# Kernel optimization log

Measured on AMD Instinct MI355X. Metric: run time of the kernel, lower is better.

The kernel has to match this reference:

```python
import jax, jax.numpy as jnp
import numpy as np

N_NODES = 100000
N_EDGES = 1600000
IN_CH = 128
DIM = 128
OUT_CH = 10
NUM_GRAPHS = 128
BN_EPS = 1e-5


def _bn_train(h, gamma, beta):
    # BatchNorm1d in training mode: batch statistics over the node axis
    mean = jnp.mean(h, axis=0)
    var = jnp.var(h, axis=0)
    return (h - mean) * jax.lax.rsqrt(var + BN_EPS) * gamma + beta


def _gin_conv(x, src, dst, W1, b1, gamma, beta, W2, b2):
    # GINConv with eps=0: nn(x + sum_{j in N(i)} x_j)
    agg = jax.ops.segment_sum(x[src], dst, num_segments=x.shape[0])  # [N, d]
    h = (x + agg) @ W1 + b1
    h = jax.nn.relu(_bn_train(h, gamma, beta))
    h = jax.nn.relu(h @ W2 + b2)
    return h


def setup_inputs() -> dict:
    key = jax.random.key(0)
    ks = jax.random.split(key, 16)
    s = 0.02
    inp = {
        "x": jax.random.normal(ks[0], (N_NODES, IN_CH), dtype=jnp.float32),
        "edge_index": jax.random.randint(ks[1], (2, N_EDGES), 0, N_NODES, dtype=jnp.int64),
        "batch": jnp.sort(jax.random.randint(ks[2], (N_NODES,), 0, NUM_GRAPHS, dtype=jnp.int64)),
        # conv1 MLP
        "W1a": jax.random.normal(ks[3], (IN_CH, DIM), dtype=jnp.float32) * s,
        "b1a": jnp.zeros((DIM,), jnp.float32),
        "ga": jnp.ones((DIM,), jnp.float32),
        "ba": jnp.zeros((DIM,), jnp.float32),
        "W2a": jax.random.normal(ks[4], (DIM, DIM), dtype=jnp.float32) * s,
        "b2a": jnp.zeros((DIM,), jnp.float32),
        # conv2 MLP
        "W1b": jax.random.normal(ks[5], (DIM, DIM), dtype=jnp.float32) * s,
        "b1b": jnp.zeros((DIM,), jnp.float32),
        "gb": jnp.ones((DIM,), jnp.float32),
        "bb": jnp.zeros((DIM,), jnp.float32),
        "W2b": jax.random.normal(ks[6], (DIM, DIM), dtype=jnp.float32) * s,
        "b2b": jnp.zeros((DIM,), jnp.float32),
        # readout linears
        "Wl1": jax.random.normal(ks[7], (DIM, DIM), dtype=jnp.float32) * s,
        "bl1": jnp.zeros((DIM,), jnp.float32),
        "Wl2": jax.random.normal(ks[8], (DIM, OUT_CH), dtype=jnp.float32) * s,
        "bl2": jnp.zeros((OUT_CH,), jnp.float32),
    }
    return inp


def reference(x, edge_index, batch, W1a, b1a, ga, ba, W2a, b2a,
              W1b, b1b, gb, bb, W2b, b2b, Wl1, bl1, Wl2, bl2):
    src, dst = edge_index[0], edge_index[1]
    h = _gin_conv(x, src, dst, W1a, b1a, ga, ba, W2a, b2a)
    h = _gin_conv(h, src, dst, W1b, b1b, gb, bb, W2b, b2b)
    pooled = jax.ops.segment_sum(h, batch, num_segments=NUM_GRAPHS)  # [G, d]
    out = jax.nn.relu(pooled @ Wl1 + bl1)
    # dropout p=0.5 is identity in deterministic/eval evaluation
    out = out @ Wl2 + bl2
    return out
```

## Files before the change

### kernel.cpp

```cpp
#include <hip/hip_runtime.h>

#define N_NODES    100000
#define N_EDGES    1600000
#define DIM        128
#define OUT_CH     10
#define NUM_GRAPHS 128
#define BN_EPS     1e-5f

#define BSHIFT   8
#define NB2      391
#define CAP2     5120
#define NTILES   782

typedef __attribute__((ext_vector_type(8))) short short8;
typedef __attribute__((ext_vector_type(4))) float floatx4;

__device__ inline float bf2f(unsigned short u) {
    union { unsigned i; float f; } v; v.i = (unsigned)u << 16; return v.f;
}
__device__ inline unsigned short f2bf(float f) {
    union { float f; unsigned i; } v; v.f = f;
    unsigned r = (v.i + 0x7fffu + ((v.i >> 16) & 1u)) >> 16;
    return (unsigned short)r;
}

__device__ inline void async_cp16(const unsigned short* g, unsigned short* l) {
    __builtin_amdgcn_global_load_lds(
        (const __attribute__((address_space(1))) void*)g,
        (__attribute__((address_space(3))) void*)l, 16, 0, 0);
}

__global__ void k_cvt_x(const float* __restrict__ x, unsigned short* __restrict__ xb,
                        int* __restrict__ gcur, float* __restrict__ stats4,
                        float* __restrict__ pooled) {
    int t = threadIdx.x;
    if (blockIdx.x == 0) {
        for (int i = t; i < NB2 + 1; i += 256) gcur[i] = 0;
        for (int i = t; i < 4 * DIM; i += 256) stats4[i] = 0.f;
        for (int i = t; i < NUM_GRAPHS * DIM; i += 256) pooled[i] = 0.f;
    }
    int idx = blockIdx.x * 256 + t;
    float4 v = ((const float4*)x)[idx];
    ushort4 o;
    o.x = f2bf(v.x); o.y = f2bf(v.y); o.z = f2bf(v.z); o.w = f2bf(v.w);
    ((ushort4*)xb)[idx] = o;
}

__global__ void k_prep_w(const float* __restrict__ W0, const float* __restrict__ W1,
                         const float* __restrict__ W2, const float* __restrict__ W3,
                         unsigned short* __restrict__ Wt) {
    const float* Ws[4] = {W0, W1, W2, W3};
    const float* W = Ws[blockIdx.y];
    unsigned short* o = Wt + blockIdx.y * (DIM * DIM);
    int idx = blockIdx.x * 256 + threadIdx.x;
    int n = idx >> 7, k = idx & 127;
    o[idx] = f2bf(W[k * DIM + n]);
}

__global__ __launch_bounds__(256)
void k_bucket(const int* __restrict__ src, const int* __restrict__ dst,
              int* __restrict__ gcur, unsigned* __restrict__ pairs) {
    __shared__ int cnt[NB2 + 1];
    __shared__ int lofs[NB2 + 1];
    __shared__ int gbase[NB2 + 1];
    __shared__ int scanA[256], scanB[256];
    __shared__ int stage[8192];

    int t = threadIdx.x;
    for (int i = t; i < NB2 + 1; i += 256) cnt[i] = 0;
    __syncthreads();
    int base = blockIdx.x * 8192;
    int n_e = min(8192, N_EDGES - base);
    for (int i = t; i < n_e; i += 256)
        atomicAdd(&cnt[dst[base + i] >> BSHIFT], 1);
    __syncthreads();
    int vA = cnt[t];
    int vB = (t < NB2 - 256) ? cnt[256 + t] : 0;
    scanA[t] = vA; scanB[t] = vB;
    __syncthreads();
    for (int off = 1; off < 256; off <<= 1) {
        int tA = (t >= off) ? scanA[t - off] : 0;
        int tB = (t >= off) ? scanB[t - off] : 0;
        __syncthreads();
        scanA[t] += tA; scanB[t] += tB;
        __syncthreads();
    }
    lofs[t] = scanA[t] - vA;
    if (t < NB2 - 256) lofs[256 + t] = scanA[255] + scanB[t] - vB;
    __syncthreads();
    for (int i = t; i < NB2; i += 256) {
        gbase[i] = (cnt[i] > 0) ? atomicAdd(&gcur[i], cnt[i]) : 0;
        cnt[i] = lofs[i];
    }
    __syncthreads();
    for (int i = t; i < n_e; i += 256) {
        int d = dst[base + i];
        int b = d >> BSHIFT;
        int pos = atomicAdd(&cnt[b], 1);
        stage[pos] = (int)(((unsigned)src[base + i] << 8) | (unsigned)(d & 255));
    }
    __syncthreads();
    int w = t >> 6, lane = t & 63;
    for (int b = w; b < NB2; b += 4) {
        int len = cnt[b] - lofs[b];
        int g0  = gbase[b];
        int maxlen = CAP2 - g0; if (maxlen < 0) maxlen = 0;
        if (len > maxlen) len = maxlen;
        unsigned* dp = pairs + (size_t)b * CAP2 + g0;
        const int* sp = stage + lofs[b];
        for (int i = lane; i < len; i += 64) dp[i] = (unsigned)sp[i];
    }
}

__global__ void k_bscan(const int* __restrict__ gcur, int* __restrict__ bbase,
                        int* __restrict__ row_ptr) {
    __shared__ int sh[512];
    int t = threadIdx.x;
    int v = (t < NB2) ? min(gcur[t], CAP2) : 0;
    sh[t] = v; __syncthreads();
    for (int off = 1; off < 512; off <<= 1) {
        int tmp = (t >= off) ? sh[t - off] : 0;
        __syncthreads();
        sh[t] += tmp;
        __syncthreads();
    }
    if (t < NB2) bbase[t] = sh[t] - v;
    if (t == NB2 - 1) { bbase[NB2] = sh[t]; row_ptr[N_NODES] = sh[t]; }
}

__global__ __launch_bounds__(256)
void k_csr(const unsigned* __restrict__ pairs, const int* __restrict__ gcur,
           const int* __restrict__ bbase, int* __restrict__ row_ptr,
           int* __restrict__ col) {
    __shared__ int hist[256];
    __shared__ int cur[256];
    __shared__ int stage[CAP2];
    int bi = blockIdx.x, t = threadIdx.x;
    hist[t] = 0; __syncthreads();
    int n = min(gcur[bi], CAP2);
    const unsigned* P = pairs + (size_t)bi * CAP2;
    for (int i = t; i < n; i += 256)
        atomicAdd(&hist[P[i] & 255u], 1);
    __syncthreads();
    int self = hist[t];
    cur[t] = self; __syncthreads();
    for (int off = 1; off < 256; off <<= 1) {
        int tmp = (t >= off) ? cur[t - off] : 0;
        __syncthreads();
        cur[t] += tmp;
        __syncthreads();
    }
    int excl = cur[t] - self;
    int base = bbase[bi];
    int node = (bi << 8) + t;
    if (node < N_NODES) row_ptr[node] = base + excl;
    cur[t] = excl;
    __syncthreads();
    for (int i = t; i < n; i += 256) {
        unsigned e = P[i];
        int pos = atomicAdd(&cur[e & 255u], 1);
        stage[pos] = (int)(e >> 8);
    }
    __syncthreads();
    for (int i = t; i < n; i += 256) col[base + i] = stage[i];
}

__global__ void k_agg(const unsigned short* __restrict__ X,
                      unsigned short* __restrict__ Out,
                      const int* __restrict__ row_ptr, const int* __restrict__ col) {
    int wid = (blockIdx.x * 256 + threadIdx.x) >> 6;
    if (wid >= N_NODES) return;
    int lane = threadIdx.x & 63;
    int half = lane >> 5, m = lane & 31;
    const ushort4* X4 = (const ushort4*)X;

    float a0=0.f,a1=0.f,a2=0.f,a3=0.f;
    float c0=0.f,c1=0.f,c2=0.f,c3=0.f;
    if (half == 0) {
        ushort4 sv = X4[(size_t)wid * 32 + m];
        a0 = bf2f(sv.x); a1 = bf2f(sv.y); a2 = bf2f(sv.z); a3 = bf2f(sv.w);
    }
    int s = row_ptr[wid], e = row_ptr[wid + 1];
    int p = s + half;
    for (; p + 6 < e; p += 8) {
        int n0 = col[p], n1 = col[p + 2], n2 = col[p + 4], n3 = col[p + 6];
        ushort4 v0 = X4[(size_t)n0 * 32 + m];
        ushort4 v1 = X4[(size_t)n1 * 32 + m];
        ushort4 v2 = X4[(size_t)n2 * 32 + m];
        ushort4 v3 = X4[(size_t)n3 * 32 + m];
        a0 += bf2f(v0.x); a1 += bf2f(v0.y); a2 += bf2f(v0.z); a3 += bf2f(v0.w);
        c0 += bf2f(v1.x); c1 += bf2f(v1.y); c2 += bf2f(v1.z); c3 += bf2f(v1.w);
        a0 += bf2f(v2.x); a1 += bf2f(v2.y); a2 += bf2f(v2.z); a3 += bf2f(v2.w);
        c0 += bf2f(v3.x); c1 += bf2f(v3.y); c2 += bf2f(v3.z); c3 += bf2f(v3.w);
    }
    for (; p < e; p += 2) {
        ushort4 v = X4[(size_t)col[p] * 32 + m];
        a0 += bf2f(v.x); a1 += bf2f(v.y); a2 += bf2f(v.z); a3 += bf2f(v.w);
    }
    a0 += c0; a1 += c1; a2 += c2; a3 += c3;
    a0 += __shfl_xor(a0, 32);
    a1 += __shfl_xor(a1, 32);
    a2 += __shfl_xor(a2, 32);
    a3 += __shfl_xor(a3, 32);
    if (half == 0) {
        ushort4 o;
        o.x = f2bf(a0); o.y = f2bf(a1); o.z = f2bf(a2); o.w = f2bf(a3);
        ((ushort4*)Out)[(size_t)wid * 32 + m] = o;
    }
}

template<bool BN_LOAD, bool STATS, bool RELU_ST>
__global__ __launch_bounds__(512)
void k_gemm(const unsigned short* __restrict__ In, unsigned short* __restrict__ Out,
            const unsigned short* __restrict__ Wt, const float* __restrict__ bias,
            const float* __restrict__ ssum_in, const float* __restrict__ ssq_in,
            const float* __restrict__ gamma, const float* __restrict__ beta,
            float* __restrict__ ssum_out, float* __restrict__ ssq_out) {
    __shared__ __align__(16) unsigned short sB[128 * 128];
    __shared__ float ssc[128], ssh[128];
    __shared__ float s_sum[128], s_sq[128];

    int t = threadIdx.x;
    int w = t >> 6, lane = t & 63;
    int tm = w >> 2, wv = w & 3;
    int m = lane & 15;
    int q = lane >> 4;
    int tile = blockIdx.x * 2 + tm;
    int r0 = tile * 128;

    int rowA0 = min(r0 + wv * 32 + m,      N_NODES - 1);
    int rowA1 = min(r0 + wv * 32 + 16 + m, N_NODES - 1);
    short8 a0[4], a1[4];
    #pragma unroll
    for (int kk = 0; kk < 4; ++kk) {
        a0[kk] = *(const short8*)(In + (size_t)rowA0 * 128 + kk * 32 + q * 8);
        a1[kk] = *(const short8*)(In + (size_t)rowA1 * 128 + kk * 32 + q * 8);
    }

    #pragma unroll
    for (int u = 0; u < 4; ++u) {
        int i = (w * 4 + u) * 64 + lane;
        int n = i >> 4, p = i & 15;
        async_cp16(Wt + n * 128 + ((p ^ (n & 7)) << 3), sB + (size_t)(w * 4 + u) * 512);
    }
    if (BN_LOAD && t < 128) {
        float mn  = ssum_in[t] * (1.0f / N_NODES);
        float var = ssq_in[t] * (1.0f / N_NODES) - mn * mn;
        float inv = rsqrtf(var + BN_EPS);
        float sc  = gamma[t] * inv;
        ssc[t] = sc; ssh[t] = beta[t] - mn * sc;
    }
    if (STATS && t < 128) { s_sum[t] = 0.f; s_sq[t] = 0.f; }
    __syncthreads();

    if (BN_LOAD) {
        #pragma unroll
        for (int kk = 0; kk < 4; ++kk) {
            int base = kk * 32 + q * 8;
            #pragma unroll
            for (int j = 0; j < 8; ++j) {
                float scj = ssc[base + j], shj = ssh[base + j];
                float f0 = fmaxf(bf2f((unsigned short)a0[kk][j]) * scj + shj, 0.f);
                float f1 = fmaxf(bf2f((unsigned short)a1[kk][j]) * scj + shj, 0.f);
                a0[kk][j] = (short)f2bf(f0);
                a1[kk][j] = (short)f2bf(f1);
            }
        }
    }

    int sw = m & 7;
    floatx4 acc[2][8] = {};
    #pragma unroll
    for (int kk = 0; kk < 4; ++kk) {
        int cp = (kk * 4 + q) ^ sw;
        #pragma unroll
        for (int c = 0; c < 8; ++c) {
            int nr = c * 16 + m;
            short8 b = *(const short8*)&sB[nr * 128 + (cp << 3)];
            acc[0][c] = __builtin_amdgcn_mfma_f32_16x16x32_bf16(b, a0[kk], acc[0][c], 0, 0, 0);
            acc[1][c] = __builtin_amdgcn_mfma_f32_16x16x32_bf16(b, a1[kk], acc[1][c], 0, 0, 0);
        }
    }

    #pragma unroll
    for (int c = 0; c < 8; ++c) {
        int ch0 = c * 16 + q * 4;
        float4 bv = *(const float4*)(bias + ch0);
        float sr[4] = {0,0,0,0}, qr[4] = {0,0,0,0};
        #pragma unroll
        for (int h = 0; h < 2; ++h) {
            int node = r0 + wv * 32 + h * 16 + m;
            float v0 = acc[h][c][0] + bv.x;
            float v1 = acc[h][c][1] + bv.y;
            float v2 = acc[h][c][2] + bv.z;
            float v3 = acc[h][c][3] + bv.w;
            if (RELU_ST) {
                v0 = fmaxf(v0, 0.f); v1 = fmaxf(v1, 0.f);
                v2 = fmaxf(v2, 0.f); v3 = fmaxf(v3, 0.f);
            }
            if (node < N_NODES) {
                ushort4 o;
                o.x = f2bf(v0); o.y = f2bf(v1); o.z = f2bf(v2); o.w = f2bf(v3);
                *(ushort4*)(Out + (size_t)node * 128 + ch0) = o;
                if (STATS) {
                    sr[0] += v0; sr[1] += v1; sr[2] += v2; sr[3] += v3;
                    qr[0] += v0*v0; qr[1] += v1*v1; qr[2] += v2*v2; qr[3] += v3*v3;
                }
            }
        }
        if (STATS) {
            #pragma unroll
            for (int msk = 1; msk <= 8; msk <<= 1) {
                #pragma unroll
                for (int r = 0; r < 4; ++r) {
                    sr[r] += __shfl_xor(sr[r], msk);
                    qr[r] += __shfl_xor(qr[r], msk);
                }
            }
            if (m == 0) {
                #pragma unroll
                for (int r = 0; r < 4; ++r) {
                    atomicAdd(&s_sum[ch0 + r], sr[r]);
                    atomicAdd(&s_sq [ch0 + r], qr[r]);
                }
            }
        }
    }
    if (STATS) {
        __syncthreads();
        if (t < 128) {
            atomicAdd(&ssum_out[t], s_sum[t]);
            atomicAdd(&ssq_out [t], s_sq[t]);
        }
    }
}

#define POOL_BLOCKS 512
#define POOL_CHUNK  196
__global__ void k_pool(const unsigned short* __restrict__ h, const int* __restrict__ batch,
                       float* __restrict__ pooled) {
    int c  = threadIdx.x;
    int n0 = blockIdx.x * POOL_CHUNK;
    if (n0 >= N_NODES) return;
    int n1 = min(n0 + POOL_CHUNK, N_NODES);
    int g = batch[n0];
    float acc = 0.f;
    for (int i = n0; i < n1; ++i) {
        int gi = batch[i];
        if (gi != g) { atomicAdd(&pooled[g * DIM + c], acc); acc = 0.f; g = gi; }
        acc += bf2f(h[(size_t)i * DIM + c]);
    }
    atomicAdd(&pooled[g * DIM + c], acc);
}

__global__ void k_readout(const float* __restrict__ pooled,
                          const float* __restrict__ Wl1, const float* __restrict__ bl1,
                          const float* __restrict__ Wl2, const float* __restrict__ bl2,
                          float* __restrict__ out) {
    __shared__ float p[128], r[128];
    int g = blockIdx.x, c = threadIdx.x;
    p[c] = pooled[g * DIM + c];
    __syncthreads();
    float s = bl1[c];
    #pragma unroll 8
    for (int k = 0; k < DIM; ++k) s += p[k] * Wl1[k * DIM + c];
    r[c] = fmaxf(s, 0.f);
    __syncthreads();
    if (c < OUT_CH) {
        float s2 = bl2[c];
        #pragma unroll 8
        for (int k = 0; k < DIM; ++k) s2 += r[k] * Wl2[k * OUT_CH + c];
        out[g * OUT_CH + c] = s2;
    }
}

extern "C" void kernel_launch(void* const* d_in, const int* in_sizes, int n_in,
                              void* d_out, int out_size, void* d_ws, size_t ws_size,
                              hipStream_t stream) {
    const float* x   = (const float*)d_in[0];
    const int*   ei  = (const int*)d_in[1];
    const int*   bat = (const int*)d_in[2];
    const float* W1a = (const float*)d_in[3];
    const float* b1a = (const float*)d_in[4];
    const float* ga  = (const float*)d_in[5];
    const float* ba  = (const float*)d_in[6];
    const float* W2a = (const float*)d_in[7];
    const float* b2a = (const float*)d_in[8];
    const float* W1b = (const float*)d_in[9];
    const float* b1b = (const float*)d_in[10];
    const float* gb  = (const float*)d_in[11];
    const float* bbt = (const float*)d_in[12];
    const float* W2b = (const float*)d_in[13];
    const float* b2b = (const float*)d_in[14];
    const float* Wl1 = (const float*)d_in[15];
    const float* bl1 = (const float*)d_in[16];
    const float* Wl2 = (const float*)d_in[17];
    const float* bl2 = (const float*)d_in[18];
    float* out = (float*)d_out;

    const int* src = ei;
    const int* dst = ei + N_EDGES;

    char* w = (char*)d_ws;
    size_t off = 0;
    auto alloc = [&](size_t bytes) -> char* {
        char* p = w + off; off += (bytes + 255) & ~(size_t)255; return p;
    };
    unsigned short* xb   = (unsigned short*)alloc((size_t)N_NODES * DIM * 2);
    unsigned short* nb0  = (unsigned short*)alloc((size_t)N_NODES * DIM * 2);
    unsigned short* nb1  = (unsigned short*)alloc((size_t)N_NODES * DIM * 2);
    unsigned short* Wtb  = (unsigned short*)alloc((size_t)4 * DIM * DIM * 2);
    unsigned* pairs = (unsigned*)alloc((size_t)NB2 * CAP2 * 4);
    int*   row_ptr = (int*)  alloc((size_t)(N_NODES + 1) * 4);
    int*   col     = (int*)  alloc((size_t)N_EDGES * 4);
    int*   gcur    = (int*)  alloc((NB2 + 1) * 4);
    int*   bbase   = (int*)  alloc((NB2 + 1) * 4);
    float* stats4  = (float*)alloc((size_t)4 * DIM * 4);
    float* pooled  = (float*)alloc((size_t)NUM_GRAPHS * DIM * 4);
    float* ssumA = stats4, *ssqA = stats4 + DIM, *ssumB = stats4 + 2*DIM, *ssqB = stats4 + 3*DIM;

    k_cvt_x<<<(N_NODES * DIM / 4) / 256, 256, 0, stream>>>(x, xb, gcur, stats4, pooled);
    k_prep_w<<<dim3(64, 4), 256, 0, stream>>>(W1a, W2a, W1b, W2b, Wtb);
    const unsigned short* Wt1a = Wtb;
    const unsigned short* Wt2a = Wtb + DIM * DIM;
    const unsigned short* Wt1b = Wtb + 2 * DIM * DIM;
    const unsigned short* Wt2b = Wtb + 3 * DIM * DIM;

    k_bucket<<<(N_EDGES + 8191) / 8192, 256, 0, stream>>>(src, dst, gcur, pairs);
    k_bscan<<<1, 512, 0, stream>>>(gcur, bbase, row_ptr);
    k_csr<<<NB2, 256, 0, stream>>>(pairs, gcur, bbase, row_ptr, col);

    int agg_blocks  = (N_NODES * 64) / 256;
    int gemm_blocks = NTILES / 2;

    k_agg<<<agg_blocks, 256, 0, stream>>>(xb, nb0, row_ptr, col);
    k_gemm<false, true, false><<<gemm_blocks, 512, 0, stream>>>(
        nb0, nb1, Wt1a, b1a, nullptr, nullptr, nullptr, nullptr, ssumA, ssqA);
    k_gemm<true, false, true><<<gemm_blocks, 512, 0, stream>>>(
        nb1, nb0, Wt2a, b2a, ssumA, ssqA, ga, ba, nullptr, nullptr);
    k_agg<<<agg_blocks, 256, 0, stream>>>(nb0, nb1, row_ptr, col);
    k_gemm<false, true, false><<<gemm_blocks, 512, 0, stream>>>(
        nb1, nb0, Wt1b, b1b, nullptr, nullptr, nullptr, nullptr, ssumB, ssqB);
    k_gemm<true, false, true><<<gemm_blocks, 512, 0, stream>>>(
        nb0, nb1, Wt2b, b2b, ssumB, ssqB, gb, bbt, nullptr, nullptr);
    k_pool<<<POOL_BLOCKS, 128, 0, stream>>>(nb1, bat, pooled);
    k_readout<<<NUM_GRAPHS, 128, 0, stream>>>(pooled, Wl1, bl1, Wl2, bl2, out);
}
```

Baseline: 495.9 us.

## Make GEMM kernel persistent with register prefetch of next tile

The row-tile GEMM becomes a persistent kernel: a fixed grid of 256 blocks of 256 threads loops over the 782 tiles. It loads the weight matrix into LDS once per block rather than once per two tiles, and prefetches the next tile's A rows into registers while computing the current one. This amortises the weight staging and overlaps global loads with MFMA work, at the cost of higher register pressure and fewer waves per block. The second half of the tail tiles may leave some CUs idle.

```diff
diff --git a/kernel.cpp b/kernel.cpp
--- a/kernel.cpp
+++ b/kernel.cpp
@@ -11,6 +11,7 @@
 #define NB2      391
 #define CAP2     5120
 #define NTILES   782
+#define GEMM_GRID 256
 
 typedef __attribute__((ext_vector_type(8))) short short8;
 typedef __attribute__((ext_vector_type(4))) float floatx4;
@@ -210,7 +211,7 @@
 }
 
 template<bool BN_LOAD, bool STATS, bool RELU_ST>
-__global__ __launch_bounds__(512)
+__global__ __launch_bounds__(256)
 void k_gemm(const unsigned short* __restrict__ In, unsigned short* __restrict__ Out,
             const unsigned short* __restrict__ Wt, const float* __restrict__ bias,
             const float* __restrict__ ssum_in, const float* __restrict__ ssq_in,
@@ -222,26 +223,15 @@
 
     int t = threadIdx.x;
     int w = t >> 6, lane = t & 63;
-    int tm = w >> 2, wv = w & 3;
     int m = lane & 15;
     int q = lane >> 4;
-    int tile = blockIdx.x * 2 + tm;
-    int r0 = tile * 128;
-
-    int rowA0 = min(r0 + wv * 32 + m,      N_NODES - 1);
-    int rowA1 = min(r0 + wv * 32 + 16 + m, N_NODES - 1);
-    short8 a0[4], a1[4];
+    int sw = m & 7;
+
     #pragma unroll
-    for (int kk = 0; kk < 4; ++kk) {
-        a0[kk] = *(const short8*)(In + (size_t)rowA0 * 128 + kk * 32 + q * 8);
-        a1[kk] = *(const short8*)(In + (size_t)rowA1 * 128 + kk * 32 + q * 8);
-    }
-
-    #pragma unroll
-    for (int u = 0; u < 4; ++u) {
-        int i = (w * 4 + u) * 64 + lane;
+    for (int u = 0; u < 8; ++u) {
+        int i = (w * 8 + u) * 64 + lane;
         int n = i >> 4, p = i & 15;
-        async_cp16(Wt + n * 128 + ((p ^ (n & 7)) << 3), sB + (size_t)(w * 4 + u) * 512);
+        async_cp16(Wt + n * 128 + ((p ^ (n & 7)) << 3), sB + (size_t)(w * 8 + u) * 512);
     }
     if (BN_LOAD && t < 128) {
         float mn  = ssum_in[t] * (1.0f / N_NODES);
@@ -251,81 +241,115 @@
         ssc[t] = sc; ssh[t] = beta[t] - mn * sc;
     }
     if (STATS && t < 128) { s_sum[t] = 0.f; s_sq[t] = 0.f; }
-    __syncthreads();
-
-    if (BN_LOAD) {
+
+    int tile = blockIdx.x;
+    short8 a0[4], a1[4];
+    {
+        int rA0 = min(tile * 128 + w * 32 + m,      N_NODES - 1);
+        int rA1 = min(tile * 128 + w * 32 + 16 + m, N_NODES - 1);
         #pragma unroll
         for (int kk = 0; kk < 4; ++kk) {
-            int base = kk * 32 + q * 8;
+            a0[kk] = *(const short8*)(In + (size_t)rA0 * 128 + kk * 32 + q * 8);
+            a1[kk] = *(const short8*)(In + (size_t)rA1 * 128 + kk * 32 + q * 8);
+        }
+    }
+    __syncthreads();
+
+    #pragma unroll 1
+    for (; tile < NTILES; ) {
+        int next = tile + GEMM_GRID;
+        short8 b0[4], b1[4];
+        if (next < NTILES) {
+            int rN0 = min(next * 128 + w * 32 + m,      N_NODES - 1);
+            int rN1 = min(next * 128 + w * 32 + 16 + m, N_NODES - 1);
             #pragma unroll
-            for (int j = 0; j < 8; ++j) {
-                float scj = ssc[base + j], shj = ssh[base + j];
-                float f0 = fmaxf(bf2f((unsigned short)a0[kk][j]) * scj + shj, 0.f);
-                float f1 = fmaxf(bf2f((unsigned short)a1[kk][j]) * scj + shj, 0.f);
-                a0[kk][j] = (short)f2bf(f0);
-                a1[kk][j] = (short)f2bf(f1);
+            for (int kk = 0; kk < 4; ++kk) {
+                b0[kk] = *(const short8*)(In + (size_t)rN0 * 128 + kk * 32 + q * 8);
+                b1[kk] = *(const short8*)(In + (size_t)rN1 * 128 + kk * 32 + q * 8);
             }
         }
-    }
-
-    int sw = m & 7;
-    floatx4 acc[2][8] = {};
-    #pragma unroll
-    for (int kk = 0; kk < 4; ++kk) {
-        int cp = (kk * 4 + q) ^ sw;
+
+        if (BN_LOAD) {
+            #pragma unroll
+            for (int kk = 0; kk < 4; ++kk) {
+                int base = kk * 32 + q * 8;
+                #pragma unroll
+                for (int j = 0; j < 8; ++j) {
+                    float scj = ssc[base + j], shj = ssh[base + j];
+                    float f0 = fmaxf(bf2f((unsigned short)a0[kk][j]) * scj + shj, 0.f);
+                    float f1 = fmaxf(bf2f((unsigned short)a1[kk][j]) * scj + shj, 0.f);
+                    a0[kk][j] = (short)f2bf(f0);
+                    a1[kk][j] = (short)f2bf(f1);
+                }
+            }
+        }
+
+        floatx4 acc[2][8] = {};
+        #pragma unroll
+        for (int kk = 0; kk < 4; ++kk) {
+            int cp = (kk * 4 + q) ^ sw;
+            #pragma unroll
+            for (int c = 0; c < 8; ++c) {
+                int nr = c * 16 + m;
+                short8 b = *(const short8*)&sB[nr * 128 + (cp << 3)];
+                acc[0][c] = __builtin_amdgcn_mfma_f32_16x16x32_bf16(b, a0[kk], acc[0][c], 0, 0, 0);
+                acc[1][c] = __builtin_amdgcn_mfma_f32_16x16x32_bf16(b, a1[kk], acc[1][c], 0, 0, 0);
+            }
+        }
+
+        int r0 = tile * 128;
         #pragma unroll
         for (int c = 0; c < 8; ++c) {
-            int nr = c * 16 + m;
-            short8 b = *(const short8*)&sB[nr * 128 + (cp << 3)];
-            acc[0][c] = __builtin_amdgcn_mfma_f32_16x16x32_bf16(b, a0[kk], acc[0][c], 0, 0, 0);
-            acc[1][c] = __builtin_amdgcn_mfma_f32_16x16x32_bf16(b, a1[kk], acc[1][c], 0, 0, 0);
-        }
-    }
-
-    #pragma unroll
-    for (int c = 0; c < 8; ++c) {
-        int ch0 = c * 16 + q * 4;
-        float4 bv = *(const float4*)(bias + ch0);
-        float sr[4] = {0,0,0,0}, qr[4] = {0,0,0,0};
-        #pragma unroll
-        for (int h = 0; h < 2; ++h) {
-            int node = r0 + wv * 32 + h * 16 + m;
-            float v0 = acc[h][c][0] + bv.x;
-            float v1 = acc[h][c][1] + bv.y;
-            float v2 = acc[h][c][2] + bv.z;
-            float v3 = acc[h][c][3] + bv.w;
-            if (RELU_ST) {
-                v0 = fmaxf(v0, 0.f); v1 = fmaxf(v1, 0.f);
-                v2 = fmaxf(v2, 0.f); v3 = fmaxf(v3, 0.f);
-            }
-            if (node < N_NODES) {
-                ushort4 o;
-                o.x = f2bf(v0); o.y = f2bf(v1); o.z = f2bf(v2); o.w = f2bf(v3);
-                *(ushort4*)(Out + (size_t)node * 128 + ch0) = o;
-                if (STATS) {
-                    sr[0] += v0; sr[1] += v1; sr[2] += v2; sr[3] += v3;
-                    qr[0] += v0*v0; qr[1] += v1*v1; qr[2] += v2*v2; qr[3] += v3*v3;
+            int ch0 = c * 16 + q * 4;
+            float4 bv = *(const float4*)(bias + ch0);
+            float sr[4] = {0,0,0,0}, qr[4] = {0,0,0,0};
+            #pragma unroll
+            for (int h = 0; h < 2; ++h) {
+                int node = r0 + w * 32 + h * 16 + m;
+                float v0 = acc[h][c][0] + bv.x;
+                float v1 = acc[h][c][1] + bv.y;
+                float v2 = acc[h][c][2] + bv.z;
+                float v3 = acc[h][c][3] + bv.w;
+                if (RELU_ST) {
+                    v0 = fmaxf(v0, 0.f); v1 = fmaxf(v1, 0.f);
+                    v2 = fmaxf(v2, 0.f); v3 = fmaxf(v3, 0.f);
+                }
+                if (node < N_NODES) {
+                    ushort4 o;
+                    o.x = f2bf(v0); o.y = f2bf(v1); o.z = f2bf(v2); o.w = f2bf(v3);
+                    *(ushort4*)(Out + (size_t)node * 128 + ch0) = o;
+                    if (STATS) {
+                        sr[0] += v0; sr[1] += v1; sr[2] += v2; sr[3] += v3;
+                        qr[0] += v0*v0; qr[1] += v1*v1; qr[2] += v2*v2; qr[3] += v3*v3;
+                    }
                 }
             }
-        }
-        if (STATS) {
-            #pragma unroll
-            for (int msk = 1; msk <= 8; msk <<= 1) {
+            if (STATS) {
                 #pragma unroll
-                for (int r = 0; r < 4; ++r) {
-                    sr[r] += __shfl_xor(sr[r], msk);
-                    qr[r] += __shfl_xor(qr[r], msk);
+                for (int msk = 1; msk <= 8; msk <<= 1) {
+                    #pragma unroll
+                    for (int r = 0; r < 4; ++r) {
+                        sr[r] += __shfl_xor(sr[r], msk);
+                        qr[r] += __shfl_xor(qr[r], msk);
+                    }
+                }
+                if (m == 0) {
+                    #pragma unroll
+                    for (int r = 0; r < 4; ++r) {
+                        atomicAdd(&s_sum[ch0 + r], sr[r]);
+                        atomicAdd(&s_sq [ch0 + r], qr[r]);
+                    }
                 }
             }
-            if (m == 0) {
-                #pragma unroll
-                for (int r = 0; r < 4; ++r) {
-                    atomicAdd(&s_sum[ch0 + r], sr[r]);
-                    atomicAdd(&s_sq [ch0 + r], qr[r]);
-                }
-            }
-        }
-    }
+        }
+
+        tile = next;
+        if (tile < NTILES) {
+            #pragma unroll
+            for (int kk = 0; kk < 4; ++kk) { a0[kk] = b0[kk]; a1[kk] = b1[kk]; }
+        }
+    }
+
     if (STATS) {
         __syncthreads();
         if (t < 128) {
@@ -430,18 +454,17 @@
     k_bscan<<<1, 512, 0, stream>>>(gcur, bbase, row_ptr);
     k_csr<<<NB2, 256, 0, stream>>>(pairs, gcur, bbase, row_ptr, col);
 
-    int agg_blocks  = (N_NODES * 64) / 256;
-    int gemm_blocks = NTILES / 2;
+    int agg_blocks = (N_NODES * 64) / 256;
 
     k_agg<<<agg_blocks, 256, 0, stream>>>(xb, nb0, row_ptr, col);
-    k_gemm<false, true, false><<<gemm_blocks, 512, 0, stream>>>(
+    k_gemm<false, true, false><<<GEMM_GRID, 256, 0, stream>>>(
         nb0, nb1, Wt1a, b1a, nullptr, nullptr, nullptr, nullptr, ssumA, ssqA);
-    k_gemm<true, false, true><<<gemm_blocks, 512, 0, stream>>>(
+    k_gemm<true, false, true><<<GEMM_GRID, 256, 0, stream>>>(
         nb1, nb0, Wt2a, b2a, ssumA, ssqA, ga, ba, nullptr, nullptr);
     k_agg<<<agg_blocks, 256, 0, stream>>>(nb0, nb1, row_ptr, col);
-    k_gemm<false, true, false><<<gemm_blocks, 512, 0, stream>>>(
+    k_gemm<false, true, false><<<GEMM_GRID, 256, 0, stream>>>(
         nb1, nb0, Wt1b, b1b, nullptr, nullptr, nullptr, nullptr, ssumB, ssqB);
-    k_gemm<true, false, true><<<gemm_blocks, 512, 0, stream>>>(
+    k_gemm<true, false, true><<<GEMM_GRID, 256, 0, stream>>>(
         nb0, nb1, Wt2b, b2b, ssumB, ssqB, gb, bbt, nullptr, nullptr);
     k_pool<<<POOL_BLOCKS, 128, 0, stream>>>(nb1, bat, pooled);
     k_readout<<<NUM_GRAPHS, 128, 0, stream>>>(pooled, Wl1, bl1, Wl2, bl2, out);
```

New measurement: 494.4 us. No clear change (-0.3%).
